# Performance work log

Hardware: AMD Instinct MI355X
Metric: run time of the kernel (lower is better)

## Reference

```python
import math
import jax, jax.numpy as jnp
import numpy as np

B, L, IN_DIM, D, OUT_DIM = 4, 4096, 512, 64, 512


def setup_inputs() -> dict:
    key = jax.random.key(0)
    ks = jax.random.split(key, 9)
    s_in = 1.0 / math.sqrt(IN_DIM)
    s_d = 1.0 / math.sqrt(D)
    return {
        "x": jax.random.normal(ks[0], (B, L, IN_DIM), jnp.float32),
        "Wq": jax.random.normal(ks[1], (IN_DIM, D), jnp.float32) * s_in,
        "bq": jax.random.normal(ks[2], (D,), jnp.float32) * s_in,
        "Wk": jax.random.normal(ks[3], (IN_DIM, D), jnp.float32) * s_in,
        "bk": jax.random.normal(ks[4], (D,), jnp.float32) * s_in,
        "Wv": jax.random.normal(ks[5], (IN_DIM, D), jnp.float32) * s_in,
        "bv": jax.random.normal(ks[6], (D,), jnp.float32) * s_in,
        "Wo": jax.random.normal(ks[7], (D, OUT_DIM), jnp.float32) * s_d,
        "bo": jax.random.normal(ks[8], (OUT_DIM,), jnp.float32) * s_d,
    }


def reference(x, Wq, bq, Wk, bk, Wv, bv, Wo, bo):
    # q, k, v: [B, L, D]
    q = x @ Wq + bq
    k = x @ Wk + bk
    v = x @ Wv + bv
    scale = 1.0 / math.sqrt(D)
    # scores: [B, Lq, Lk]
    scores = jnp.einsum("bqd,bkd->bqk", q, k) * scale
    # NOTE: original uses nn.Softmax(dim=1) -> softmax over the QUERY axis (axis=1)
    attention = jax.nn.softmax(scores, axis=1)
    values_with_attention = jnp.einsum("bqk,bkd->bqd", attention, v)
    output = values_with_attention @ Wo + bo
    return (output, attention)
```

## Files before the change

### kernel.cpp

```cpp
#include <hip/hip_runtime.h>
#include <hip/hip_fp16.h>
#include <math.h>

#define Bdim 4
#define Lseq 4096
#define INDIM 512
#define DH 64
#define OUTD 512
#define SCALE 0.125f
#define KSPL 8
#define QSPL 4
#define BL (Bdim * Lseq)

typedef _Float16 f16;
typedef _Float16 h8 __attribute__((ext_vector_type(8)));
typedef float f4 __attribute__((ext_vector_type(4)));

#define MFMA(a, b, c) __builtin_amdgcn_mfma_f32_16x16x32_f16(a, b, c, 0, 0, 0)

__global__ __launch_bounds__(256) void proj_qkv(const float* __restrict__ x,
                                                const float* __restrict__ Wq,
                                                const float* __restrict__ bq,
                                                const float* __restrict__ Wk,
                                                const float* __restrict__ bk,
                                                const float* __restrict__ Wv,
                                                const float* __restrict__ bv,
                                                f16* __restrict__ qh,
                                                f16* __restrict__ kh,
                                                f16* __restrict__ vt) {
    __shared__ float xT[64 * 68];
    __shared__ float Ws[3][64 * 68];
    int t = threadIdx.x;
    int row0 = blockIdx.x * 64;
    int r4 = t >> 4, c4 = t & 15;
    float acc[3][4][4] = {};
    for (int kc = 0; kc < INDIM; kc += 64) {
        __syncthreads();
        {
            int row = t >> 2, kq = (t & 3) * 16;
            const float4* src = (const float4*)(x + (size_t)(row0 + row) * INDIM + kc + kq);
            float tmp[16];
#pragma unroll
            for (int i = 0; i < 4; ++i) {
                float4 v = src[i];
                tmp[4*i+0] = v.x; tmp[4*i+1] = v.y; tmp[4*i+2] = v.z; tmp[4*i+3] = v.w;
            }
#pragma unroll
            for (int j = 0; j < 16; ++j) xT[(kq + j) * 68 + row] = tmp[j];
        }
        {
            int k = t >> 2, dq = (t & 3) * 16;
            const float4* sq = (const float4*)(Wq + (size_t)(kc + k) * DH + dq);
            const float4* sk = (const float4*)(Wk + (size_t)(kc + k) * DH + dq);
            const float4* sv = (const float4*)(Wv + (size_t)(kc + k) * DH + dq);
#pragma unroll
            for (int i = 0; i < 4; ++i) {
                *(float4*)(&Ws[0][k * 68 + dq + 4 * i]) = sq[i];
                *(float4*)(&Ws[1][k * 68 + dq + 4 * i]) = sk[i];
                *(float4*)(&Ws[2][k * 68 + dq + 4 * i]) = sv[i];
            }
        }
        __syncthreads();
#pragma unroll 4
        for (int k = 0; k < 64; ++k) {
            f4 xv = *(f4*)(xT + k * 68 + r4 * 4);
            f4 w0 = *(f4*)(&Ws[0][k * 68 + c4 * 4]);
            f4 w1 = *(f4*)(&Ws[1][k * 68 + c4 * 4]);
            f4 w2 = *(f4*)(&Ws[2][k * 68 + c4 * 4]);
#pragma unroll
            for (int i = 0; i < 4; ++i)
#pragma unroll
                for (int j = 0; j < 4; ++j) {
                    acc[0][i][j] += xv[i] * w0[j];
                    acc[1][i][j] += xv[i] * w1[j];
                    acc[2][i][j] += xv[i] * w2[j];
                }
        }
    }
#pragma unroll
    for (int i = 0; i < 4; ++i) {
        size_t row = row0 + r4 * 4 + i;
#pragma unroll
        for (int j = 0; j < 4; ++j) {
            int d = c4 * 4 + j;
            qh[row * DH + d] = (f16)((acc[0][i][j] + bq[d]) * SCALE);
            kh[row * DH + d] = (f16)(acc[1][i][j] + bk[d]);
        }
    }
    __syncthreads();
#pragma unroll
    for (int i = 0; i < 4; ++i)
#pragma unroll
        for (int j = 0; j < 4; ++j)
            xT[(c4 * 4 + j) * 68 + r4 * 4 + i] = acc[2][i][j] + bv[c4 * 4 + j];
    __syncthreads();
    {
        int b = row0 >> 12;
        int krow = row0 & (Lseq - 1);
        int d = t >> 2, kq = (t & 3) * 16;
#pragma unroll
        for (int i = 0; i < 2; ++i) {
            h8 pack;
#pragma unroll
            for (int j = 0; j < 8; ++j) pack[j] = (f16)xT[d * 68 + kq + i * 8 + j];
            *(h8*)(vt + ((size_t)b * DH + d) * Lseq + krow + kq + i * 8) = pack;
        }
    }
}

__global__ __launch_bounds__(256) void col_stats(const f16* __restrict__ qh,
                                                 const f16* __restrict__ kh,
                                                 float* __restrict__ lsum) {
    __shared__ __align__(16) f16 qlds[32 * 72];
    int t = threadIdx.x;
    int w = t >> 6, lane = t & 63;
    int l15 = lane & 15, quad = lane >> 4;
    int b = blockIdx.y;
    int kblk = blockIdx.x * 64;
    int qbase = blockIdx.z * (Lseq / QSPL);

    int krow = kblk + w * 16 + l15;
    const h8* kr = (const h8*)(kh + ((size_t)b * Lseq + krow) * DH + quad * 8);
    h8 a0 = kr[0];
    h8 a1 = kr[4];
    float lp[4] = {0.f, 0.f, 0.f, 0.f};

    for (int qs = 0; qs < Lseq / QSPL; qs += 32) {
        __syncthreads();
        {
            int row = t >> 3, c8 = t & 7;
            *(h8*)(qlds + row * 72 + c8 * 8) =
                *(const h8*)(qh + ((size_t)b * Lseq + qbase + qs + row) * DH + c8 * 8);
        }
        __syncthreads();
#pragma unroll
        for (int nt = 0; nt < 2; ++nt) {
            const f16* qp = qlds + (nt * 16 + l15) * 72 + quad * 8;
            h8 b0 = *(const h8*)qp;
            h8 b1 = *(const h8*)(qp + 32);
            f4 c = {0.f, 0.f, 0.f, 0.f};
            c = MFMA(a0, b0, c);
            c = MFMA(a1, b1, c);
#pragma unroll
            for (int reg = 0; reg < 4; ++reg) lp[reg] += __expf(c[reg]);
        }
    }
#pragma unroll
    for (int reg = 0; reg < 4; ++reg) {
        float v = lp[reg];
        v += __shfl_xor(v, 1);
        v += __shfl_xor(v, 2);
        v += __shfl_xor(v, 4);
        v += __shfl_xor(v, 8);
        if (l15 == 0)
            atomicAdd(&lsum[(size_t)b * Lseq + kblk + w * 16 + quad * 4 + reg], v);
    }
}

__global__ __launch_bounds__(256) void attn_pv(const f16* __restrict__ qh,
                                               const f16* __restrict__ kh,
                                               const f16* __restrict__ vt,
                                               const float* __restrict__ lsum,
                                               float* __restrict__ att,
                                               f16* __restrict__ opart) {
    __shared__ __align__(16) f16 klds[64 * 72];
    __shared__ __align__(16) float es[4][32 * 76];
    int t = threadIdx.x;
    int w = t >> 6, lane = t & 63;
    int l15 = lane & 15, quad = lane >> 4;
    int b = blockIdx.y;
    int q0 = blockIdx.x * 128 + w * 32;
    int split = blockIdx.z;

    h8 aq[2][2];
#pragma unroll
    for (int mt = 0; mt < 2; ++mt) {
        const h8* qp = (const h8*)(qh + ((size_t)b * Lseq + q0 + mt * 16 + l15) * DH + quad * 8);
        aq[mt][0] = qp[0];
        aq[mt][1] = qp[4];
    }
    f4 o[2][4];
#pragma unroll
    for (int mt = 0; mt < 2; ++mt)
#pragma unroll
        for (int nt = 0; nt < 4; ++nt) o[mt][nt] = (f4){0.f, 0.f, 0.f, 0.f};

    const float* lsb = lsum + (size_t)b * Lseq;
    float* ew = es[w];

    for (int kt = 0; kt < Lseq / KSPL; kt += 64) {
        int kbase = split * (Lseq / KSPL) + kt;
        __syncthreads();
#pragma unroll
        for (int i = 0; i < 2; ++i) {
            int lin = i * 256 + t;
            int row = lin >> 3, c8 = lin & 7;
            *(h8*)(klds + row * 72 + c8 * 8) =
                *(const h8*)(kh + ((size_t)b * Lseq + kbase + row) * DH + c8 * 8);
        }
        __syncthreads();

        h8 bk[4][2];
        float rlv[4];
#pragma unroll
        for (int nt = 0; nt < 4; ++nt) {
            const f16* kp = klds + (nt * 16 + l15) * 72 + quad * 8;
            bk[nt][0] = *(const h8*)kp;
            bk[nt][1] = *(const h8*)(kp + 32);
            rlv[nt] = 1.0f / lsb[kbase + nt * 16 + l15];
        }

#pragma unroll
        for (int mt = 0; mt < 2; ++mt)
#pragma unroll
            for (int nt = 0; nt < 4; ++nt) {
                f4 c = {0.f, 0.f, 0.f, 0.f};
                c = MFMA(aq[mt][0], bk[nt][0], c);
                c = MFMA(aq[mt][1], bk[nt][1], c);
#pragma unroll
                for (int reg = 0; reg < 4; ++reg) {
                    float a = __expf(c[reg]) * rlv[nt];
                    ew[(mt * 16 + quad * 4 + reg) * 76 + nt * 16 + l15] = a;
                }
            }

        {
            int r = lane >> 4;
            int cc = (lane & 15) * 4;
#pragma unroll
            for (int i = 0; i < 8; ++i) {
                int row = i * 4 + r;
                f4 v = *(const f4*)(ew + row * 76 + cc);
                *(f4*)(att + ((size_t)b * Lseq + q0 + row) * Lseq + kbase + cc) = v;
            }
        }

        h8 ae[2][2];
#pragma unroll
        for (int mt = 0; mt < 2; ++mt) {
            const float* ep = ew + (mt * 16 + l15) * 76 + quad * 8;
            f4 x0 = *(const f4*)ep;
            f4 x1 = *(const f4*)(ep + 4);
            f4 y0 = *(const f4*)(ep + 32);
            f4 y1 = *(const f4*)(ep + 36);
            h8 h0, h1;
#pragma unroll
            for (int j = 0; j < 4; ++j) {
                h0[j] = (f16)x0[j]; h0[4 + j] = (f16)x1[j];
                h1[j] = (f16)y0[j]; h1[4 + j] = (f16)y1[j];
            }
            ae[mt][0] = h0;
            ae[mt][1] = h1;
        }
#pragma unroll
        for (int nt = 0; nt < 4; ++nt) {
            const h8* vp = (const h8*)(vt + ((size_t)b * DH + nt * 16 + l15) * Lseq + kbase + quad * 8);
            h8 bv0 = vp[0];
            h8 bv1 = vp[4];
            o[0][nt] = MFMA(ae[0][0], bv0, o[0][nt]);
            o[0][nt] = MFMA(ae[0][1], bv1, o[0][nt]);
            o[1][nt] = MFMA(ae[1][0], bv0, o[1][nt]);
            o[1][nt] = MFMA(ae[1][1], bv1, o[1][nt]);
        }
    }

#pragma unroll
    for (int mt = 0; mt < 2; ++mt)
#pragma unroll
        for (int nt = 0; nt < 4; ++nt)
#pragma unroll
            for (int reg = 0; reg < 4; ++reg) {
                size_t qrow = (size_t)b * Lseq + q0 + mt * 16 + quad * 4 + reg;
                opart[((size_t)split * BL + qrow) * DH + nt * 16 + l15] = (f16)o[mt][nt][reg];
            }
}

#define WOFF(c) ((c) * 8 + ((c) >> 2) * 4)

__global__ __launch_bounds__(256) void out_proj(const f16* __restrict__ opart,
                                                const float* __restrict__ Wo,
                                                const float* __restrict__ bo,
                                                float* __restrict__ out) {
    __shared__ float osT[64 * 68];
    __shared__ float wos[64 * 144];
    int t = threadIdx.x;
    int rg = blockIdx.x, oq = blockIdx.y;
#pragma unroll
    for (int j = 0; j < 8; ++j) {
        int idx = j * 256 + t;
        int dd = idx >> 5, c4b = idx & 31;
        int c8b = c4b >> 1, half = (c4b & 1) * 4;
        *(float4*)(wos + dd * 144 + WOFF(c8b) + half) =
            *(const float4*)(Wo + (size_t)dd * OUTD + oq * 128 + c4b * 4);
    }
    {
        int row = t >> 2, dq = (t & 3) * 16;
        float s[16] = {};
#pragma unroll
        for (int sp = 0; sp < KSPL; ++sp) {
            const h8* src = (const h8*)(opart + ((size_t)sp * BL + (size_t)rg * 64 + row) * DH + dq);
            h8 v0 = src[0], v1 = src[1];
#pragma unroll
            for (int jj = 0; jj < 8; ++jj) {
                s[jj] += (float)v0[jj];
                s[8 + jj] += (float)v1[jj];
            }
        }
#pragma unroll
        for (int jj = 0; jj < 16; ++jj) osT[(dq + jj) * 68 + row] = s[jj];
    }
    __syncthreads();
    int r4 = t >> 4, c8 = t & 15;
    float acc[4][8] = {};
#pragma unroll 8
    for (int dd = 0; dd < DH; ++dd) {
        f4 ov = *(f4*)(osT + dd * 68 + r4 * 4);
        f4 w0 = *(f4*)(wos + dd * 144 + WOFF(c8));
        f4 w1 = *(f4*)(wos + dd * 144 + WOFF(c8) + 4);
#pragma unroll
        for (int i = 0; i < 4; ++i)
#pragma unroll
            for (int j = 0; j < 4; ++j) {
                acc[i][j]     += ov[i] * w0[j];
                acc[i][4 + j] += ov[i] * w1[j];
            }
    }
    f4 b0 = *(const f4*)(bo + oq * 128 + c8 * 8);
    f4 b1 = *(const f4*)(bo + oq * 128 + c8 * 8 + 4);
#pragma unroll
    for (int i = 0; i < 4; ++i) {
        size_t row = (size_t)rg * 64 + r4 * 4 + i;
        f4 r0, r1;
#pragma unroll
        for (int j = 0; j < 4; ++j) {
            r0[j] = acc[i][j] + b0[j];
            r1[j] = acc[i][4 + j] + b1[j];
        }
        *(f4*)(out + row * OUTD + oq * 128 + c8 * 8) = r0;
        *(f4*)(out + row * OUTD + oq * 128 + c8 * 8 + 4) = r1;
    }
}

extern "C" void kernel_launch(void* const* d_in, const int* in_sizes, int n_in,
                              void* d_out, int out_size, void* d_ws, size_t ws_size,
                              hipStream_t stream) {
    const float* x  = (const float*)d_in[0];
    const float* Wq = (const float*)d_in[1];
    const float* bq = (const float*)d_in[2];
    const float* Wk = (const float*)d_in[3];
    const float* bk = (const float*)d_in[4];
    const float* Wv = (const float*)d_in[5];
    const float* bv = (const float*)d_in[6];
    const float* Wo = (const float*)d_in[7];
    const float* bo = (const float*)d_in[8];

    float* out = (float*)d_out;
    float* att = out + (size_t)BL * OUTD;

    char* ws = (char*)d_ws;
    f16*   qh    = (f16*)(ws + 0);
    f16*   kh    = (f16*)(ws + (size_t)(2 << 20));
    f16*   vt    = (f16*)(ws + (size_t)(4 << 20));
    float* lsum  = (float*)(ws + (size_t)(6 << 20));
    f16*   opart = (f16*)(ws + (size_t)(7 << 20));

    hipMemsetAsync(lsum, 0, (size_t)BL * sizeof(float), stream);
    proj_qkv<<<dim3(BL / 64), 256, 0, stream>>>(x, Wq, bq, Wk, bk, Wv, bv, qh, kh, vt);
    col_stats<<<dim3(Lseq / 64, Bdim, QSPL), 256, 0, stream>>>(qh, kh, lsum);
    attn_pv<<<dim3(Lseq / 128, Bdim, KSPL), 256, 0, stream>>>(qh, kh, vt, lsum, att, opart);
    out_proj<<<dim3(BL / 64, OUTD / 128), 256, 0, stream>>>(opart, Wo, bo, out);
}
```

Measured before the change: 476.2 us.

## Double-buffer K/Q tiles, fp16 score staging, retile projection and column-stats kernels

```diff
diff --git a/kernel.cpp b/kernel.cpp
--- a/kernel.cpp
+++ b/kernel.cpp
@@ -9,16 +9,17 @@
 #define OUTD 512
 #define SCALE 0.125f
 #define KSPL 8
-#define QSPL 4
+#define QSPL 8
 #define BL (Bdim * Lseq)
 
 typedef _Float16 f16;
 typedef _Float16 h8 __attribute__((ext_vector_type(8)));
 typedef float f4 __attribute__((ext_vector_type(4)));
+typedef float f2 __attribute__((ext_vector_type(2)));
 
 #define MFMA(a, b, c) __builtin_amdgcn_mfma_f32_16x16x32_f16(a, b, c, 0, 0, 0)
 
-__global__ __launch_bounds__(256) void proj_qkv(const float* __restrict__ x,
+__global__ __launch_bounds__(512) void proj_qkv(const float* __restrict__ x,
                                                 const float* __restrict__ Wq,
                                                 const float* __restrict__ bq,
                                                 const float* __restrict__ Wk,
@@ -32,29 +33,29 @@
     __shared__ float Ws[3][64 * 68];
     int t = threadIdx.x;
     int row0 = blockIdx.x * 64;
-    int r4 = t >> 4, c4 = t & 15;
-    float acc[3][4][4] = {};
+    int r2 = t >> 4, c4 = t & 15;
+    float acc[3][2][4] = {};
     for (int kc = 0; kc < INDIM; kc += 64) {
         __syncthreads();
         {
-            int row = t >> 2, kq = (t & 3) * 16;
+            int row = t >> 3, kq = (t & 7) * 8;
             const float4* src = (const float4*)(x + (size_t)(row0 + row) * INDIM + kc + kq);
-            float tmp[16];
-#pragma unroll
-            for (int i = 0; i < 4; ++i) {
+            float tmp[8];
+#pragma unroll
+            for (int i = 0; i < 2; ++i) {
                 float4 v = src[i];
                 tmp[4*i+0] = v.x; tmp[4*i+1] = v.y; tmp[4*i+2] = v.z; tmp[4*i+3] = v.w;
             }
 #pragma unroll
-            for (int j = 0; j < 16; ++j) xT[(kq + j) * 68 + row] = tmp[j];
+            for (int j = 0; j < 8; ++j) xT[(kq + j) * 68 + row] = tmp[j];
         }
         {
-            int k = t >> 2, dq = (t & 3) * 16;
+            int k = t >> 3, dq = (t & 7) * 8;
             const float4* sq = (const float4*)(Wq + (size_t)(kc + k) * DH + dq);
             const float4* sk = (const float4*)(Wk + (size_t)(kc + k) * DH + dq);
             const float4* sv = (const float4*)(Wv + (size_t)(kc + k) * DH + dq);
 #pragma unroll
-            for (int i = 0; i < 4; ++i) {
+            for (int i = 0; i < 2; ++i) {
                 *(float4*)(&Ws[0][k * 68 + dq + 4 * i]) = sq[i];
                 *(float4*)(&Ws[1][k * 68 + dq + 4 * i]) = sk[i];
                 *(float4*)(&Ws[2][k * 68 + dq + 4 * i]) = sv[i];
@@ -63,12 +64,12 @@
         __syncthreads();
 #pragma unroll 4
         for (int k = 0; k < 64; ++k) {
-            f4 xv = *(f4*)(xT + k * 68 + r4 * 4);
+            f2 xv = *(f2*)(xT + k * 68 + r2 * 2);
             f4 w0 = *(f4*)(&Ws[0][k * 68 + c4 * 4]);
             f4 w1 = *(f4*)(&Ws[1][k * 68 + c4 * 4]);
             f4 w2 = *(f4*)(&Ws[2][k * 68 + c4 * 4]);
 #pragma unroll
-            for (int i = 0; i < 4; ++i)
+            for (int i = 0; i < 2; ++i)
 #pragma unroll
                 for (int j = 0; j < 4; ++j) {
                     acc[0][i][j] += xv[i] * w0[j];
@@ -78,8 +79,8 @@
         }
     }
 #pragma unroll
-    for (int i = 0; i < 4; ++i) {
-        size_t row = row0 + r4 * 4 + i;
+    for (int i = 0; i < 2; ++i) {
+        size_t row = row0 + r2 * 2 + i;
 #pragma unroll
         for (int j = 0; j < 4; ++j) {
             int d = c4 * 4 + j;
@@ -89,88 +90,112 @@
     }
     __syncthreads();
 #pragma unroll
-    for (int i = 0; i < 4; ++i)
+    for (int i = 0; i < 2; ++i)
 #pragma unroll
         for (int j = 0; j < 4; ++j)
-            xT[(c4 * 4 + j) * 68 + r4 * 4 + i] = acc[2][i][j] + bv[c4 * 4 + j];
+            xT[(c4 * 4 + j) * 68 + r2 * 2 + i] = acc[2][i][j] + bv[c4 * 4 + j];
     __syncthreads();
     {
         int b = row0 >> 12;
         int krow = row0 & (Lseq - 1);
-        int d = t >> 2, kq = (t & 3) * 16;
-#pragma unroll
-        for (int i = 0; i < 2; ++i) {
-            h8 pack;
-#pragma unroll
-            for (int j = 0; j < 8; ++j) pack[j] = (f16)xT[d * 68 + kq + i * 8 + j];
-            *(h8*)(vt + ((size_t)b * DH + d) * Lseq + krow + kq + i * 8) = pack;
-        }
+        int d = t >> 3, kq = (t & 7) * 8;
+        h8 pack;
+#pragma unroll
+        for (int j = 0; j < 8; ++j) pack[j] = (f16)xT[d * 68 + kq + j];
+        *(h8*)(vt + ((size_t)b * DH + d) * Lseq + krow + kq) = pack;
     }
 }
 
 __global__ __launch_bounds__(256) void col_stats(const f16* __restrict__ qh,
                                                  const f16* __restrict__ kh,
                                                  float* __restrict__ lsum) {
-    __shared__ __align__(16) f16 qlds[32 * 72];
+    __shared__ __align__(16) f16 qlds[2][64 * 72];
     int t = threadIdx.x;
     int w = t >> 6, lane = t & 63;
     int l15 = lane & 15, quad = lane >> 4;
     int b = blockIdx.y;
-    int kblk = blockIdx.x * 64;
+    int kblk = blockIdx.x * 128;
     int qbase = blockIdx.z * (Lseq / QSPL);
 
-    int krow = kblk + w * 16 + l15;
-    const h8* kr = (const h8*)(kh + ((size_t)b * Lseq + krow) * DH + quad * 8);
-    h8 a0 = kr[0];
-    h8 a1 = kr[4];
-    float lp[4] = {0.f, 0.f, 0.f, 0.f};
-
-    for (int qs = 0; qs < Lseq / QSPL; qs += 32) {
-        __syncthreads();
-        {
-            int row = t >> 3, c8 = t & 7;
-            *(h8*)(qlds + row * 72 + c8 * 8) =
-                *(const h8*)(qh + ((size_t)b * Lseq + qbase + qs + row) * DH + c8 * 8);
-        }
-        __syncthreads();
-#pragma unroll
-        for (int nt = 0; nt < 2; ++nt) {
-            const f16* qp = qlds + (nt * 16 + l15) * 72 + quad * 8;
+    h8 a[2][2];
+#pragma unroll
+    for (int kt = 0; kt < 2; ++kt) {
+        const h8* kr = (const h8*)(kh + ((size_t)b * Lseq + kblk + w * 32 + kt * 16 + l15) * DH + quad * 8);
+        a[kt][0] = kr[0];
+        a[kt][1] = kr[4];
+    }
+    float lp[2][4] = {};
+
+#pragma unroll
+    for (int i = 0; i < 2; ++i) {
+        int lin = i * 256 + t;
+        int row = lin >> 3, c8 = lin & 7;
+        *(h8*)(qlds[0] + row * 72 + c8 * 8) =
+            *(const h8*)(qh + ((size_t)b * Lseq + qbase + row) * DH + c8 * 8);
+    }
+    __syncthreads();
+
+    for (int it = 0; it < (Lseq / QSPL) / 64; ++it) {
+        h8 s0, s1;
+        int r0_ = 0, c0_ = 0, r1_ = 0, c1_ = 0;
+        if (it < 7) {
+            int lin0 = t, lin1 = 256 + t;
+            r0_ = lin0 >> 3; c0_ = lin0 & 7;
+            r1_ = lin1 >> 3; c1_ = lin1 & 7;
+            s0 = *(const h8*)(qh + ((size_t)b * Lseq + qbase + (it + 1) * 64 + r0_) * DH + c0_ * 8);
+            s1 = *(const h8*)(qh + ((size_t)b * Lseq + qbase + (it + 1) * 64 + r1_) * DH + c1_ * 8);
+        }
+        const f16* qb = qlds[it & 1];
+#pragma unroll
+        for (int nt = 0; nt < 4; ++nt) {
+            const f16* qp = qb + (nt * 16 + l15) * 72 + quad * 8;
             h8 b0 = *(const h8*)qp;
             h8 b1 = *(const h8*)(qp + 32);
-            f4 c = {0.f, 0.f, 0.f, 0.f};
-            c = MFMA(a0, b0, c);
-            c = MFMA(a1, b1, c);
-#pragma unroll
-            for (int reg = 0; reg < 4; ++reg) lp[reg] += __expf(c[reg]);
-        }
-    }
-#pragma unroll
-    for (int reg = 0; reg < 4; ++reg) {
-        float v = lp[reg];
-        v += __shfl_xor(v, 1);
-        v += __shfl_xor(v, 2);
-        v += __shfl_xor(v, 4);
-        v += __shfl_xor(v, 8);
-        if (l15 == 0)
-            atomicAdd(&lsum[(size_t)b * Lseq + kblk + w * 16 + quad * 4 + reg], v);
-    }
+#pragma unroll
+            for (int kt = 0; kt < 2; ++kt) {
+                f4 c = {0.f, 0.f, 0.f, 0.f};
+                c = MFMA(a[kt][0], b0, c);
+                c = MFMA(a[kt][1], b1, c);
+#pragma unroll
+                for (int reg = 0; reg < 4; ++reg) lp[kt][reg] += __expf(c[reg]);
+            }
+        }
+        if (it < 7) {
+            f16* qn = qlds[(it & 1) ^ 1];
+            *(h8*)(qn + r0_ * 72 + c0_ * 8) = s0;
+            *(h8*)(qn + r1_ * 72 + c1_ * 8) = s1;
+        }
+        __syncthreads();
+    }
+#pragma unroll
+    for (int kt = 0; kt < 2; ++kt)
+#pragma unroll
+        for (int reg = 0; reg < 4; ++reg) {
+            float v = lp[kt][reg];
+            v += __shfl_xor(v, 1);
+            v += __shfl_xor(v, 2);
+            v += __shfl_xor(v, 4);
+            v += __shfl_xor(v, 8);
+            if (l15 == 0)
+                atomicAdd(&lsum[(size_t)b * Lseq + kblk + w * 32 + kt * 16 + quad * 4 + reg], v);
+        }
 }
 
-__global__ __launch_bounds__(256) void attn_pv(const f16* __restrict__ qh,
-                                               const f16* __restrict__ kh,
-                                               const f16* __restrict__ vt,
-                                               const float* __restrict__ lsum,
-                                               float* __restrict__ att,
-                                               f16* __restrict__ opart) {
-    __shared__ __align__(16) f16 klds[64 * 72];
-    __shared__ __align__(16) float es[4][32 * 76];
+__global__ __launch_bounds__(256, 4) void attn_pv(const f16* __restrict__ qh,
+                                                  const f16* __restrict__ kh,
+                                                  const f16* __restrict__ vt,
+                                                  const float* __restrict__ lsum,
+                                                  float* __restrict__ att,
+                                                  f16* __restrict__ opart) {
+    __shared__ __align__(16) f16 klds[2][64 * 72];
+    __shared__ __align__(16) f16 es[4][32 * 80];
     int t = threadIdx.x;
     int w = t >> 6, lane = t & 63;
     int l15 = lane & 15, quad = lane >> 4;
     int b = blockIdx.y;
     int q0 = blockIdx.x * 128 + w * 32;
     int split = blockIdx.z;
+    int kstart = split * (Lseq / KSPL);
 
     h8 aq[2][2];
 #pragma unroll
@@ -186,71 +211,73 @@
         for (int nt = 0; nt < 4; ++nt) o[mt][nt] = (f4){0.f, 0.f, 0.f, 0.f};
 
     const float* lsb = lsum + (size_t)b * Lseq;
-    float* ew = es[w];
-
-    for (int kt = 0; kt < Lseq / KSPL; kt += 64) {
-        int kbase = split * (Lseq / KSPL) + kt;
-        __syncthreads();
-#pragma unroll
-        for (int i = 0; i < 2; ++i) {
-            int lin = i * 256 + t;
-            int row = lin >> 3, c8 = lin & 7;
-            *(h8*)(klds + row * 72 + c8 * 8) =
-                *(const h8*)(kh + ((size_t)b * Lseq + kbase + row) * DH + c8 * 8);
-        }
-        __syncthreads();
-
-        h8 bk[4][2];
-        float rlv[4];
+    f16* ew = es[w];
+
+#pragma unroll
+    for (int i = 0; i < 2; ++i) {
+        int lin = i * 256 + t;
+        int row = lin >> 3, c8 = lin & 7;
+        *(h8*)(klds[0] + row * 72 + c8 * 8) =
+            *(const h8*)(kh + ((size_t)b * Lseq + kstart + row) * DH + c8 * 8);
+    }
+    __syncthreads();
+
+    for (int it = 0; it < 8; ++it) {
+        int kbase = kstart + it * 64;
+        const f16* kb = klds[it & 1];
+
+        h8 s0, s1;
+        int r0_ = 0, c0_ = 0, r1_ = 0, c1_ = 0;
+        if (it < 7) {
+            int lin0 = t, lin1 = 256 + t;
+            r0_ = lin0 >> 3; c0_ = lin0 & 7;
+            r1_ = lin1 >> 3; c1_ = lin1 & 7;
+            s0 = *(const h8*)(kh + ((size_t)b * Lseq + kbase + 64 + r0_) * DH + c0_ * 8);
+            s1 = *(const h8*)(kh + ((size_t)b * Lseq + kbase + 64 + r1_) * DH + c1_ * 8);
+        }
+
 #pragma unroll
         for (int nt = 0; nt < 4; ++nt) {
-            const f16* kp = klds + (nt * 16 + l15) * 72 + quad * 8;
-            bk[nt][0] = *(const h8*)kp;
-            bk[nt][1] = *(const h8*)(kp + 32);
-            rlv[nt] = 1.0f / lsb[kbase + nt * 16 + l15];
-        }
-
-#pragma unroll
-        for (int mt = 0; mt < 2; ++mt)
-#pragma unroll
-            for (int nt = 0; nt < 4; ++nt) {
+            const f16* kp = kb + (nt * 16 + l15) * 72 + quad * 8;
+            h8 b0 = *(const h8*)kp;
+            h8 b1 = *(const h8*)(kp + 32);
+            float rlv = 1.0f / lsb[kbase + nt * 16 + l15];
+#pragma unroll
+            for (int mt = 0; mt < 2; ++mt) {
                 f4 c = {0.f, 0.f, 0.f, 0.f};
-                c = MFMA(aq[mt][0], bk[nt][0], c);
-                c = MFMA(aq[mt][1], bk[nt][1], c);
-#pragma unroll
-                for (int reg = 0; reg < 4; ++reg) {
-                    float a = __expf(c[reg]) * rlv[nt];
-                    ew[(mt * 16 + quad * 4 + reg) * 76 + nt * 16 + l15] = a;
+                c = MFMA(aq[mt][0], b0, c);
+                c = MFMA(aq[mt][1], b1, c);
+#pragma unroll
+                for (int reg = 0; reg < 4; ++reg)
+                    ew[(mt * 16 + quad * 4 + reg) * 80 + nt * 16 + l15] =
+                        (f16)(__expf(c[reg]) * rlv);
+            }
+        }
+
+        {
+            int g = lane >> 3, c8 = lane & 7;
+#pragma unroll
+            for (int rr = 0; rr < 4; ++rr) {
+                int row = rr * 8 + g;
+                h8 hv = *(const h8*)(ew + row * 80 + c8 * 8);
+                f4 v0, v1;
+#pragma unroll
+                for (int j = 0; j < 4; ++j) {
+                    v0[j] = (float)hv[j];
+                    v1[j] = (float)hv[4 + j];
                 }
-            }
-
-        {
-            int r = lane >> 4;
-            int cc = (lane & 15) * 4;
-#pragma unroll
-            for (int i = 0; i < 8; ++i) {
-                int row = i * 4 + r;
-                f4 v = *(const f4*)(ew + row * 76 + cc);
-                *(f4*)(att + ((size_t)b * Lseq + q0 + row) * Lseq + kbase + cc) = v;
+                float* dst = att + ((size_t)b * Lseq + q0 + row) * Lseq + kbase + c8 * 8;
+                *(f4*)dst = v0;
+                *(f4*)(dst + 4) = v1;
             }
         }
 
         h8 ae[2][2];
 #pragma unroll
         for (int mt = 0; mt < 2; ++mt) {
-            const float* ep = ew + (mt * 16 + l15) * 76 + quad * 8;
-            f4 x0 = *(const f4*)ep;
-            f4 x1 = *(const f4*)(ep + 4);
-            f4 y0 = *(const f4*)(ep + 32);
-            f4 y1 = *(const f4*)(ep + 36);
-            h8 h0, h1;
-#pragma unroll
-            for (int j = 0; j < 4; ++j) {
-                h0[j] = (f16)x0[j]; h0[4 + j] = (f16)x1[j];
-                h1[j] = (f16)y0[j]; h1[4 + j] = (f16)y1[j];
-            }
-            ae[mt][0] = h0;
-            ae[mt][1] = h1;
+            const f16* ep = ew + (mt * 16 + l15) * 80 + quad * 8;
+            ae[mt][0] = *(const h8*)ep;
+            ae[mt][1] = *(const h8*)(ep + 32);
         }
 #pragma unroll
         for (int nt = 0; nt < 4; ++nt) {
@@ -262,6 +289,13 @@
             o[1][nt] = MFMA(ae[1][0], bv0, o[1][nt]);
             o[1][nt] = MFMA(ae[1][1], bv1, o[1][nt]);
         }
+
+        if (it < 7) {
+            f16* kn = klds[(it & 1) ^ 1];
+            *(h8*)(kn + r0_ * 72 + c0_ * 8) = s0;
+            *(h8*)(kn + r1_ * 72 + c1_ * 8) = s1;
+        }
+        __syncthreads();
     }
 
 #pragma unroll
@@ -365,8 +399,8 @@
     f16*   opart = (f16*)(ws + (size_t)(7 << 20));
 
     hipMemsetAsync(lsum, 0, (size_t)BL * sizeof(float), stream);
-    proj_qkv<<<dim3(BL / 64), 256, 0, stream>>>(x, Wq, bq, Wk, bk, Wv, bv, qh, kh, vt);
-    col_stats<<<dim3(Lseq / 64, Bdim, QSPL), 256, 0, stream>>>(qh, kh, lsum);
+    proj_qkv<<<dim3(BL / 64), 512, 0, stream>>>(x, Wq, bq, Wk, bk, Wv, bv, qh, kh, vt);
+    col_stats<<<dim3(Lseq / 128, Bdim, QSPL), 256, 0, stream>>>(qh, kh, lsum);
     attn_pv<<<dim3(Lseq / 128, Bdim, KSPL), 256, 0, stream>>>(qh, kh, vt, lsum, att, opart);
     out_proj<<<dim3(BL / 64, OUTD / 128), 256, 0, stream>>>(opart, Wo, bo, out);
 }
```

Measured after the change: 452.5 us. -5.0%, faster.
